# Kernel optimization log

Measured on AMD Instinct MI355X. Metric: run time of the kernel, lower is better.

Reference implementation:

```python
import jax, jax.numpy as jnp
import numpy as np

D_MODEL = 4096
N_CHUNKS = 8
CHUNK = D_MODEL // N_CHUNKS
EPS = 1e-5


def setup_inputs() -> dict:
    key = jax.random.key(0)
    k = jax.random.split(key, 5)
    B, L = 4, 4096
    x = jax.random.normal(k[0], (B, L, D_MODEL), dtype=jnp.float32)
    # kaiming_uniform with a=sqrt(5) on [n,c,c]: fan_in = c, bound = 1/sqrt(fan_in)
    bound = 1.0 / np.sqrt(CHUNK)
    w1 = jax.random.uniform(k[1], (N_CHUNKS, CHUNK, CHUNK), jnp.float32, -bound, bound)
    w2 = jax.random.uniform(k[2], (N_CHUNKS, CHUNK, CHUNK), jnp.float32, -bound, bound)
    b1 = jnp.zeros((N_CHUNKS, CHUNK), jnp.float32)
    b2 = jnp.zeros((N_CHUNKS, CHUNK), jnp.float32)
    ln_g = jnp.ones((D_MODEL,), jnp.float32)
    ln_b = jnp.zeros((D_MODEL,), jnp.float32)
    return {"x": x, "w1": w1, "b1": b1, "w2": w2, "b2": b2, "ln_g": ln_g, "ln_b": ln_b}


def reference(x, w1, b1, w2, b2, ln_g, ln_b):
    B, L, d = x.shape
    xc = x.reshape(B, L, N_CHUNKS, CHUNK)
    h = jnp.einsum('blnc,ncd->blnd', xc, w1) + b1
    h = jax.nn.gelu(h, approximate=False)  # torch F.gelu default is exact erf
    h = jnp.einsum('blnc,ncd->blnd', h, w2) + b2
    out = h.reshape(B, L, d) + x  # dropout p=0.0 -> identity
    mu = jnp.mean(out, axis=-1, keepdims=True)
    var = jnp.var(out, axis=-1, keepdims=True)
    return (out - mu) * jax.lax.rsqrt(var + EPS) * ln_g + ln_b
```

## Files before the change

### kernel.cpp

```cpp
#include <hip/hip_runtime.h>
#include <hip/hip_bf16.h>

#define TOKENS 16384
#define DMODEL 4096
#define NCH 8
#define CH 512
#define BM 64

typedef short s16x8 __attribute__((ext_vector_type(8)));
typedef float f32x4 __attribute__((ext_vector_type(4)));

__device__ __forceinline__ unsigned short f2bf(float f) {
    unsigned u = __float_as_uint(f);
    u += 0x7fffu + ((u >> 16) & 1u);
    return (unsigned short)(u >> 16);
}

__global__ __launch_bounds__(256)
void wprep_kernel(const float* __restrict__ w1, const float* __restrict__ w2,
                  unsigned short* __restrict__ p1, unsigned short* __restrict__ p2)
{
    const int lane = threadIdx.x;
    const int sub  = threadIdx.y;
    const int kt   = blockIdx.x;
    const int nb   = blockIdx.y * 4 + sub;
    const int which = blockIdx.z >> 3;
    const int n     = blockIdx.z & 7;

    const int kg  = lane >> 4;
    const int l15 = lane & 15;

    const float* src = (which ? w2 : w1) + (size_t)n * CH * CH;
    unsigned short* dst = (which ? p2 : p1) + (size_t)n * CH * CH
                        + ((size_t)(kt * 32 + nb) * 64 + lane) * 8;

    unsigned short v[8];
#pragma unroll
    for (int j = 0; j < 8; ++j)
        v[j] = f2bf(src[(size_t)(kt * 32 + kg * 8 + j) * CH + nb * 16 + l15]);

    uint4 q;
    q.x = (unsigned)v[0] | ((unsigned)v[1] << 16);
    q.y = (unsigned)v[2] | ((unsigned)v[3] << 16);
    q.z = (unsigned)v[4] | ((unsigned)v[5] << 16);
    q.w = (unsigned)v[6] | ((unsigned)v[7] << 16);
    *(uint4*)dst = q;
}

__device__ __forceinline__ void gemm_chunk(
    const unsigned short* __restrict__ wp,
    const unsigned char* lds,
    int wid, int lane, int l15, int kg,
    f32x4 (&acc)[4][8])
{
    s16x8 b0[8], b1[8], a[4];
    auto loadB = [&](s16x8 (&d)[8], int kt) {
#pragma unroll
        for (int ni = 0; ni < 8; ++ni)
            d[ni] = *(const s16x8*)(wp + ((size_t)(kt * 32 + wid * 8 + ni) * 64 + lane) * 8);
    };
    auto loadA = [&](s16x8 (&d)[4], int kt) {
#pragma unroll
        for (int mi = 0; mi < 4; ++mi) {
            int r = mi * 16 + l15;
            int byte = ((r * CH + kt * 32 + kg * 8) * 2) ^ ((r & 7) << 4);
            d[mi] = *(const s16x8*)(lds + byte);
        }
    };
    auto mm = [&](s16x8 (&aa)[4], s16x8 (&b)[8]) {
#pragma unroll
        for (int ni = 0; ni < 8; ++ni)
#pragma unroll
            for (int mi = 0; mi < 4; ++mi)
                acc[mi][ni] = __builtin_amdgcn_mfma_f32_16x16x32_bf16(aa[mi], b[ni], acc[mi][ni], 0, 0, 0);
    };

    loadB(b0, 0);
#pragma unroll 1
    for (int k2 = 0; k2 < 8; ++k2) {
        loadB(b1, 2 * k2 + 1);
        loadA(a, 2 * k2);
        mm(a, b0);
        if (k2 < 7) loadB(b0, 2 * k2 + 2);
        loadA(a, 2 * k2 + 1);
        mm(a, b1);
    }
}

__global__ __launch_bounds__(256, 2)
void mlp_kernel(const float* __restrict__ x,
                const unsigned short* __restrict__ p1,
                const unsigned short* __restrict__ p2,
                const float* __restrict__ b1,
                const float* __restrict__ b2,
                float* __restrict__ mid)
{
    __shared__ unsigned char lds[BM * CH * 2];
    const int tile = blockIdx.x;
    const int n    = blockIdx.y;
    const int tid  = threadIdx.x;
    const int wid  = tid >> 6;
    const int lane = tid & 63;
    const int row0 = tile * BM;

    {
        const float* xc = x + (size_t)row0 * DMODEL + n * CH;
#pragma unroll
        for (int it = 0; it < 32; ++it) {
            int f = it * 256 + tid;
            int r = f >> 7;
            int c = (f & 127) << 2;
            const float4 v = *(const float4*)(xc + (size_t)r * DMODEL + c);
            unsigned lo = (unsigned)f2bf(v.x) | ((unsigned)f2bf(v.y) << 16);
            unsigned hi = (unsigned)f2bf(v.z) | ((unsigned)f2bf(v.w) << 16);
            int byte = ((r * CH + c) * 2) ^ ((r & 7) << 4);
            *(uint2*)(lds + byte) = make_uint2(lo, hi);
        }
    }
    __syncthreads();

    const int nwoff = wid * 128;
    const int l15   = lane & 15;
    const int kg    = lane >> 4;

    float b1v[8], b2v[8];
#pragma unroll
    for (int ni = 0; ni < 8; ++ni) {
        int col = nwoff + ni * 16 + l15;
        b1v[ni] = b1[n * CH + col];
        b2v[ni] = b2[n * CH + col];
    }

    f32x4 acc[4][8];
#pragma unroll
    for (int mi = 0; mi < 4; ++mi)
#pragma unroll
        for (int ni = 0; ni < 8; ++ni)
            acc[mi][ni] = (f32x4){0.f, 0.f, 0.f, 0.f};

    gemm_chunk(p1 + (size_t)n * CH * CH, lds, wid, lane, l15, kg, acc);

    __syncthreads();

#pragma unroll
    for (int mi = 0; mi < 4; ++mi)
#pragma unroll
        for (int ni = 0; ni < 8; ++ni)
#pragma unroll
            for (int r = 0; r < 4; ++r) {
                float v = acc[mi][ni][r] + b1v[ni];
                v = 0.5f * v * (1.0f + erff(v * 0.70710678118654752f));
                int row  = mi * 16 + kg * 4 + r;
                int col  = nwoff + ni * 16 + l15;
                int byte = ((row * CH + col) * 2) ^ ((row & 7) << 4);
                *(unsigned short*)(lds + byte) = f2bf(v);
            }
    __syncthreads();

#pragma unroll
    for (int mi = 0; mi < 4; ++mi)
#pragma unroll
        for (int ni = 0; ni < 8; ++ni)
            acc[mi][ni] = (f32x4){0.f, 0.f, 0.f, 0.f};

    gemm_chunk(p2 + (size_t)n * CH * CH, lds, wid, lane, l15, kg, acc);

    const float* xr = x   + (size_t)row0 * DMODEL + n * CH;
    float*       mr = mid + (size_t)row0 * DMODEL + n * CH;
#pragma unroll
    for (int mi = 0; mi < 4; ++mi)
#pragma unroll
        for (int ni = 0; ni < 8; ++ni)
#pragma unroll
            for (int r = 0; r < 4; ++r) {
                int row = mi * 16 + kg * 4 + r;
                int col = nwoff + ni * 16 + l15;
                float v = acc[mi][ni][r] + b2v[ni] + xr[(size_t)row * DMODEL + col];
                mr[(size_t)row * DMODEL + col] = v;
            }
}

__global__ __launch_bounds__(256)
void ln_kernel(float* __restrict__ out,
               const float* __restrict__ g,
               const float* __restrict__ bt)
{
    __shared__ float red[8];
    const int row = blockIdx.x;
    const int tid = threadIdx.x;
    float* p = out + (size_t)row * DMODEL;

    float4 v[4];
    float s = 0.f, ss = 0.f;
#pragma unroll
    for (int i = 0; i < 4; ++i) {
        v[i] = *(const float4*)(p + (i * 256 + tid) * 4);
        s  += v[i].x + v[i].y + v[i].z + v[i].w;
        ss += v[i].x * v[i].x + v[i].y * v[i].y + v[i].z * v[i].z + v[i].w * v[i].w;
    }
#pragma unroll
    for (int o = 32; o > 0; o >>= 1) {
        s  += __shfl_xor(s, o, 64);
        ss += __shfl_xor(ss, o, 64);
    }
    const int wid = tid >> 6, lane = tid & 63;
    if (lane == 0) { red[wid] = s; red[4 + wid] = ss; }
    __syncthreads();
    s  = red[0] + red[1] + red[2] + red[3];
    ss = red[4] + red[5] + red[6] + red[7];
    const float mu   = s * (1.f / DMODEL);
    const float var  = ss * (1.f / DMODEL) - mu * mu;
    const float rstd = rsqrtf(var + 1e-5f);

#pragma unroll
    for (int i = 0; i < 4; ++i) {
        int c = (i * 256 + tid) * 4;
        float4 gv = *(const float4*)(g + c);
        float4 bv = *(const float4*)(bt + c);
        float4 o;
        o.x = (v[i].x - mu) * rstd * gv.x + bv.x;
        o.y = (v[i].y - mu) * rstd * gv.y + bv.y;
        o.z = (v[i].z - mu) * rstd * gv.z + bv.z;
        o.w = (v[i].w - mu) * rstd * gv.w + bv.w;
        *(float4*)(p + c) = o;
    }
}

extern "C" void kernel_launch(void* const* d_in, const int* in_sizes, int n_in,
                              void* d_out, int out_size, void* d_ws, size_t ws_size,
                              hipStream_t stream)
{
    const float* x    = (const float*)d_in[0];
    const float* w1   = (const float*)d_in[1];
    const float* b1   = (const float*)d_in[2];
    const float* w2   = (const float*)d_in[3];
    const float* b2   = (const float*)d_in[4];
    const float* ln_g = (const float*)d_in[5];
    const float* ln_b = (const float*)d_in[6];
    float* out = (float*)d_out;

    unsigned short* p1 = (unsigned short*)d_ws;
    unsigned short* p2 = p1 + (size_t)NCH * CH * CH;

    wprep_kernel<<<dim3(16, 8, 16), dim3(64, 4), 0, stream>>>(w1, w2, p1, p2);
    mlp_kernel<<<dim3(TOKENS / BM, NCH), dim3(256), 0, stream>>>(x, p1, p2, b1, b2, out);
    ln_kernel<<<dim3(TOKENS), dim3(256), 0, stream>>>(out, ln_g, ln_b);
}
```

Before: 360.0 us.

## Split chunk GEMMs into column halves, deepen B prefetch, use tanh GELU

Each wave's 128-column output is now computed in two 64-column halves with a 4x4 accumulator instead of 4x8. This roughly halves accumulator register pressure and frees room for three-deep B-fragment prefetch. The first half's GELU result is packed into registers while the second half computes, then both halves are written to LDS after the barrier. Exact erf GELU is replaced by a tanh-style approximation using exp and a reciprocal. That approximation departs from the exact-erf reference and may add error, alongside the extra prefetch scheduling complexity.

```diff
diff --git a/kernel.cpp b/kernel.cpp
--- a/kernel.cpp
+++ b/kernel.cpp
@@ -14,6 +14,12 @@
     unsigned u = __float_as_uint(f);
     u += 0x7fffu + ((u >> 16) & 1u);
     return (unsigned short)(u >> 16);
+}
+
+__device__ __forceinline__ float gelu_fast(float x) {
+    float u = 1.5957691216057308f * x * (1.0f + 0.044715f * x * x);
+    float e = __expf(u);
+    return x - x * __builtin_amdgcn_rcpf(e + 1.0f);
 }
 
 __global__ __launch_bounds__(256)
@@ -47,43 +53,60 @@
     *(uint4*)dst = q;
 }
 
-__device__ __forceinline__ void gemm_chunk(
+template<int DEPTH>
+__device__ __forceinline__ void gemm_half(
     const unsigned short* __restrict__ wp,
     const unsigned char* lds,
-    int wid, int lane, int l15, int kg,
-    f32x4 (&acc)[4][8])
-{
-    s16x8 b0[8], b1[8], a[4];
-    auto loadB = [&](s16x8 (&d)[8], int kt) {
-#pragma unroll
-        for (int ni = 0; ni < 8; ++ni)
-            d[ni] = *(const s16x8*)(wp + ((size_t)(kt * 32 + wid * 8 + ni) * 64 + lane) * 8);
+    int nbase,
+    int lane, int l15, int kg,
+    f32x4 (&acc)[4][4])
+{
+    s16x8 b0[4], b1[4], b2[4], a[4];
+    auto loadB = [&](s16x8 (&d)[4], int kt) {
+        const unsigned short* p = wp + ((size_t)(kt * 32 + nbase) * 64 + lane) * 8;
+#pragma unroll
+        for (int ni = 0; ni < 4; ++ni)
+            d[ni] = *(const s16x8*)(p + (size_t)ni * 64 * 8);
     };
-    auto loadA = [&](s16x8 (&d)[4], int kt) {
+    auto loadA = [&](int kt) {
 #pragma unroll
         for (int mi = 0; mi < 4; ++mi) {
             int r = mi * 16 + l15;
             int byte = ((r * CH + kt * 32 + kg * 8) * 2) ^ ((r & 7) << 4);
-            d[mi] = *(const s16x8*)(lds + byte);
+            a[mi] = *(const s16x8*)(lds + byte);
         }
     };
-    auto mm = [&](s16x8 (&aa)[4], s16x8 (&b)[8]) {
-#pragma unroll
-        for (int ni = 0; ni < 8; ++ni)
+    auto mm = [&](s16x8 (&b)[4]) {
+#pragma unroll
+        for (int ni = 0; ni < 4; ++ni)
 #pragma unroll
             for (int mi = 0; mi < 4; ++mi)
-                acc[mi][ni] = __builtin_amdgcn_mfma_f32_16x16x32_bf16(aa[mi], b[ni], acc[mi][ni], 0, 0, 0);
+                acc[mi][ni] = __builtin_amdgcn_mfma_f32_16x16x32_bf16(a[mi], b[ni], acc[mi][ni], 0, 0, 0);
     };
 
-    loadB(b0, 0);
+    if constexpr (DEPTH == 3) {
+        loadB(b0, 0); loadB(b1, 1); loadB(b2, 2);
 #pragma unroll 1
-    for (int k2 = 0; k2 < 8; ++k2) {
-        loadB(b1, 2 * k2 + 1);
-        loadA(a, 2 * k2);
-        mm(a, b0);
-        if (k2 < 7) loadB(b0, 2 * k2 + 2);
-        loadA(a, 2 * k2 + 1);
-        mm(a, b1);
+        for (int k3 = 0; k3 < 4; ++k3) {
+            const int k = k3 * 3;
+            loadA(k);     mm(b0); loadB(b0, k + 3);
+            loadA(k + 1); mm(b1); loadB(b1, k + 4);
+            loadA(k + 2); mm(b2); loadB(b2, k + 5);
+        }
+        loadA(12); mm(b0); loadB(b0, 15);
+        loadA(13); mm(b1);
+        loadA(14); mm(b2);
+        loadA(15); mm(b0);
+    } else {
+        loadB(b0, 0); loadB(b1, 1);
+#pragma unroll 1
+        for (int k2 = 0; k2 < 7; ++k2) {
+            const int k = k2 * 2;
+            loadA(k);     mm(b0); loadB(b0, k + 2);
+            loadA(k + 1); mm(b1); loadB(b1, k + 3);
+        }
+        loadA(14); mm(b0);
+        loadA(15); mm(b1);
     }
 }
 
@@ -125,59 +148,94 @@
 
     float b1v[8], b2v[8];
 #pragma unroll
-    for (int ni = 0; ni < 8; ++ni) {
-        int col = nwoff + ni * 16 + l15;
-        b1v[ni] = b1[n * CH + col];
-        b2v[ni] = b2[n * CH + col];
-    }
-
-    f32x4 acc[4][8];
+    for (int h = 0; h < 2; ++h)
+#pragma unroll
+        for (int ni = 0; ni < 4; ++ni) {
+            int col = n * CH + nwoff + h * 64 + ni * 16 + l15;
+            b1v[h * 4 + ni] = b1[col];
+            b2v[h * 4 + ni] = b2[col];
+        }
+
+    const unsigned short* p1n = p1 + (size_t)n * CH * CH;
+    const unsigned short* p2n = p2 + (size_t)n * CH * CH;
+
+    f32x4 acc[4][4];
+    auto zacc = [&]() {
+#pragma unroll
+        for (int mi = 0; mi < 4; ++mi)
+#pragma unroll
+            for (int ni = 0; ni < 4; ++ni)
+                acc[mi][ni] = (f32x4){0.f, 0.f, 0.f, 0.f};
+    };
+
+    zacc();
+    gemm_half<3>(p1n, lds, wid * 8 + 0, lane, l15, kg, acc);
+
+    unsigned g0[4][4][2];
 #pragma unroll
     for (int mi = 0; mi < 4; ++mi)
 #pragma unroll
-        for (int ni = 0; ni < 8; ++ni)
-            acc[mi][ni] = (f32x4){0.f, 0.f, 0.f, 0.f};
-
-    gemm_chunk(p1 + (size_t)n * CH * CH, lds, wid, lane, l15, kg, acc);
+        for (int ni = 0; ni < 4; ++ni)
+#pragma unroll
+            for (int j = 0; j < 2; ++j) {
+                float v0 = gelu_fast(acc[mi][ni][2 * j]     + b1v[ni]);
+                float v1 = gelu_fast(acc[mi][ni][2 * j + 1] + b1v[ni]);
+                g0[mi][ni][j] = (unsigned)f2bf(v0) | ((unsigned)f2bf(v1) << 16);
+            }
+
+    zacc();
+    gemm_half<2>(p1n, lds, wid * 8 + 4, lane, l15, kg, acc);
 
     __syncthreads();
 
 #pragma unroll
     for (int mi = 0; mi < 4; ++mi)
 #pragma unroll
-        for (int ni = 0; ni < 8; ++ni)
+        for (int ni = 0; ni < 4; ++ni)
+#pragma unroll
+            for (int j = 0; j < 2; ++j) {
+                int col  = nwoff + ni * 16 + l15;
+                int row  = mi * 16 + kg * 4 + 2 * j;
+                int byte0 = ((row * CH + col) * 2) ^ ((row & 7) << 4);
+                *(unsigned short*)(lds + byte0) = (unsigned short)(g0[mi][ni][j] & 0xffff);
+                int row1 = row + 1;
+                int byte1 = ((row1 * CH + col) * 2) ^ ((row1 & 7) << 4);
+                *(unsigned short*)(lds + byte1) = (unsigned short)(g0[mi][ni][j] >> 16);
+            }
+#pragma unroll
+    for (int mi = 0; mi < 4; ++mi)
+#pragma unroll
+        for (int ni = 0; ni < 4; ++ni)
 #pragma unroll
             for (int r = 0; r < 4; ++r) {
-                float v = acc[mi][ni][r] + b1v[ni];
-                v = 0.5f * v * (1.0f + erff(v * 0.70710678118654752f));
+                float v = gelu_fast(acc[mi][ni][r] + b1v[4 + ni]);
+                int col  = nwoff + 64 + ni * 16 + l15;
                 int row  = mi * 16 + kg * 4 + r;
-                int col  = nwoff + ni * 16 + l15;
                 int byte = ((row * CH + col) * 2) ^ ((row & 7) << 4);
                 *(unsigned short*)(lds + byte) = f2bf(v);
             }
     __syncthreads();
 
-#pragma unroll
-    for (int mi = 0; mi < 4; ++mi)
-#pragma unroll
-        for (int ni = 0; ni < 8; ++ni)
-            acc[mi][ni] = (f32x4){0.f, 0.f, 0.f, 0.f};
-
-    gemm_chunk(p2 + (size_t)n * CH * CH, lds, wid, lane, l15, kg, acc);
-
     const float* xr = x   + (size_t)row0 * DMODEL + n * CH;
     float*       mr = mid + (size_t)row0 * DMODEL + n * CH;
-#pragma unroll
-    for (int mi = 0; mi < 4; ++mi)
-#pragma unroll
-        for (int ni = 0; ni < 8; ++ni)
-#pragma unroll
-            for (int r = 0; r < 4; ++r) {
-                int row = mi * 16 + kg * 4 + r;
-                int col = nwoff + ni * 16 + l15;
-                float v = acc[mi][ni][r] + b2v[ni] + xr[(size_t)row * DMODEL + col];
-                mr[(size_t)row * DMODEL + col] = v;
-            }
+
+#pragma unroll
+    for (int h = 0; h < 2; ++h) {
+        zacc();
+        if (h == 0) gemm_half<3>(p2n, lds, wid * 8 + 0, lane, l15, kg, acc);
+        else        gemm_half<3>(p2n, lds, wid * 8 + 4, lane, l15, kg, acc);
+#pragma unroll
+        for (int mi = 0; mi < 4; ++mi)
+#pragma unroll
+            for (int ni = 0; ni < 4; ++ni)
+#pragma unroll
+                for (int r = 0; r < 4; ++r) {
+                    int row = mi * 16 + kg * 4 + r;
+                    int col = nwoff + h * 64 + ni * 16 + l15;
+                    float v = acc[mi][ni][r] + b2v[h * 4 + ni] + xr[(size_t)row * DMODEL + col];
+                    mr[(size_t)row * DMODEL + col] = v;
+                }
+    }
 }
 
 __global__ __launch_bounds__(256)
```

Result: faster. 339.8 us (-5.6%).
